# Kernel optimization log

Hardware: AMD Instinct MI355X
Metric: run time of the kernel (lower is better)

## Reference

```python
import jax, jax.numpy as jnp
import numpy as np
from jax import lax

B, L, C, H, W = 16, 8, 64, 50, 50
OC, K, PAD = 64, 3, 1
CQ = C // 16


def conv2d(x, w, b, pad):
    y = lax.conv_general_dilated(x, w, (1, 1), [(pad, pad), (pad, pad)],
                                 dimension_numbers=('NCHW', 'OIHW', 'NCHW'))
    return y + b[None, :, None, None]


def attention(x, y, q_w, q_b, k_w, k_b, v_w, v_b):
    # x, y: [b, C, 5, 5]
    b, c, h, w = x.shape
    q = conv2d(x, q_w, q_b, 1).reshape(b, -1, h * w)   # [b, CQ, N]
    kk = conv2d(y, k_w, k_b, 1).reshape(b, -1, h * w)  # [b, CQ, N]
    attn = jax.nn.softmax(jnp.einsum('bcn,bcm->bnm', q, kk), axis=-1)  # [b, Nq, Nk]
    v = conv2d(y, v_w, v_b, 1).reshape(b, c, h * w)    # [b, C, N]
    out = jnp.einsum('bcm,bnm->bcn', v, attn)          # bmm(V, attn^T)
    return out.reshape(b, c, h, w)


def setup_inputs():
    key = jax.random.key(0)
    ks = jax.random.split(key, 15)
    s = 0.05
    return {
        'x': jax.random.normal(ks[0], (B, L, C, H, W), jnp.float32),
        'weight': jax.random.normal(ks[1], (OC, C, K, K), jnp.float32) * s,
        'bias': jax.random.normal(ks[2], (OC,), jnp.float32) * s,
        'init_w': jax.random.normal(ks[3], (C, C, 3, 3), jnp.float32) * s,
        'init_b': jax.random.normal(ks[4], (C,), jnp.float32) * s,
        'q_w': jax.random.normal(ks[5], (CQ, C, 3, 3), jnp.float32) * s,
        'q_b': jax.random.normal(ks[6], (CQ,), jnp.float32) * s,
        'k_w': jax.random.normal(ks[7], (CQ, C, 3, 3), jnp.float32) * s,
        'k_b': jax.random.normal(ks[8], (CQ,), jnp.float32) * s,
        'v_w': jax.random.normal(ks[9], (C, C, 3, 3), jnp.float32) * s,
        'v_b': jax.random.normal(ks[10], (C,), jnp.float32) * s,
        'tconv_w': jax.random.normal(ks[11], (C, C), jnp.float32) * s,  # 1x1x1 Conv3d C->C
        'tconv_b': jax.random.normal(ks[12], (C,), jnp.float32) * s,
        'fc_w': jax.random.normal(ks[13], (C,), jnp.float32) * s,       # 1x1x1 Conv3d C->1
        'fc_b': jax.random.normal(ks[14], (), jnp.float32) * s,
    }


def reference(x, weight, bias, init_w, init_b, q_w, q_b, k_w, k_b, v_w, v_b,
              tconv_w, tconv_b, fc_w, fc_b):
    b, l, c, h, w = x.shape
    # --- generateweight ---
    xet = jnp.transpose(x, (0, 2, 1, 3, 4))  # [b, c, l, h, w]
    # AdaptiveMaxPool3d((None,5,5)); h,w multiples of 5 -> exact reshape max
    pooled = xet.reshape(b, c, l, 5, h // 5, 5, w // 5).max((4, 6))  # [b,c,l,5,5]
    seq = jnp.moveaxis(pooled, 2, 0)  # [l, b, c, 5, 5]
    prior0 = conv2d(seq[0], init_w, init_b, 1)

    def step(prior, xt):
        new = attention(prior, xt, q_w, q_b, k_w, k_b, v_w, v_b)
        return new, new

    _, allp = lax.scan(step, prior0, seq)            # [l, b, c, 5, 5]
    avg = jnp.moveaxis(allp, 0, 2).mean((3, 4))      # AdaptiveAvgPool3d -> [b, c, l]
    calib = jnp.einsum('oc,bcl->bol', tconv_w, avg) + tconv_b[None, :, None]  # [b,c,l]
    scale = 1.0 + jnp.transpose(calib, (0, 2, 1))    # [b, l, c]
    # finalweight[b,l,o,i,kh,kw] = weight[o,i,kh,kw] * scale[b,l,i]
    fw = weight[None, None] * scale[:, :, None, :, None, None]
    fc_out = jnp.einsum('c,bcl->bl', fc_w, avg) + fc_b  # [b, l]
    fb = bias[None, None, :] * (1.0 + fc_out)[:, :, None]  # [b, l, oc]
    # --- grouped conv with groups = b*l ---
    xg = x.reshape(1, b * l * c, h, w)
    wg = fw.reshape(b * l * OC, c, K, K)
    out = lax.conv_general_dilated(xg, wg, (1, 1), [(PAD, PAD), (PAD, PAD)],
                                   feature_group_count=b * l,
                                   dimension_numbers=('NCHW', 'OIHW', 'NCHW'))
    out = out.reshape(b * l, OC, out.shape[-2], out.shape[-1])
    out = out + fb.reshape(b * l, OC)[:, :, None, None]
    return out
```

## Files before the change

### kernel.cpp

```cpp
#include <hip/hip_runtime.h>

typedef short s16x8 __attribute__((ext_vector_type(8)));
typedef float f32x4 __attribute__((ext_vector_type(4)));
typedef unsigned int u32x4 __attribute__((ext_vector_type(4)));

__device__ __forceinline__ unsigned short bf16r(float f) {
  unsigned int u = __float_as_uint(f);
  u += 0x7fffu + ((u >> 16) & 1u);
  return (unsigned short)(u >> 16);
}
__device__ __forceinline__ float bf_lo(unsigned int u) {
  return __uint_as_float(u << 16);
}
__device__ __forceinline__ float bf_hi(unsigned int u) {
  return __uint_as_float(u & 0xffff0000u);
}


__global__ __launch_bounds__(256) void poolprep2_kernel(
    const float* __restrict__ x, float* __restrict__ pooled,
    unsigned short* __restrict__ xs) {
  const int blk = blockIdx.x;
  const int g = blk / 10;
  const int rem = blk % 10;
  const int band = rem >> 1;
  const int chalf = rem & 1;
  const int ch0 = chalf * 4;
  const float* xg = x + (size_t)g * 160000;
  unsigned short* xsg = xs + (size_t)g * (52 * 52 * 64);
  __shared__ float pm2[32 * 250];
  const int tid = threadIdx.x;

  for (int task = tid; task < 1000; task += 256) {
    int chunk4 = task & 3;
    int rest = task >> 2;
    int xpair = rest % 25;
    int r = rest / 25;
    int y = band * 10 + r;
    int chunk = ch0 + chunk4;
    const float* base = xg + (chunk * 8) * 2500 + y * 50 + xpair * 2;
    float2 v[8];
#pragma unroll
    for (int k = 0; k < 8; ++k) v[k] = *(const float2*)(base + k * 2500);
#pragma unroll
    for (int k = 0; k < 8; ++k)
      pm2[(chunk4 * 8 + k) * 250 + r * 25 + xpair] = fmaxf(v[k].x, v[k].y);
    uint4 a, b;
    a.x = (unsigned)bf16r(v[0].x) | ((unsigned)bf16r(v[1].x) << 16);
    a.y = (unsigned)bf16r(v[2].x) | ((unsigned)bf16r(v[3].x) << 16);
    a.z = (unsigned)bf16r(v[4].x) | ((unsigned)bf16r(v[5].x) << 16);
    a.w = (unsigned)bf16r(v[6].x) | ((unsigned)bf16r(v[7].x) << 16);
    b.x = (unsigned)bf16r(v[0].y) | ((unsigned)bf16r(v[1].y) << 16);
    b.y = (unsigned)bf16r(v[2].y) | ((unsigned)bf16r(v[3].y) << 16);
    b.z = (unsigned)bf16r(v[4].y) | ((unsigned)bf16r(v[5].y) << 16);
    b.w = (unsigned)bf16r(v[6].y) | ((unsigned)bf16r(v[7].y) << 16);
    int xx = xpair * 2;
    *(uint4*)&xsg[(((y + 1) * 52) + (xx + 1)) * 64 + chunk * 8] = a;
    *(uint4*)&xsg[(((y + 1) * 52) + (xx + 2)) * 64 + chunk * 8] = b;
  }
  uint4 z4;
  z4.x = 0; z4.y = 0; z4.z = 0; z4.w = 0;
  for (int task = tid; task < 80; task += 256) {
    int chunk4 = task & 3;
    int rest = task >> 2;
    int col = (rest & 1) ? 51 : 0;
    int r = rest >> 1;
    int y = band * 10 + r;
    *(uint4*)&xsg[(((y + 1) * 52) + col) * 64 + (ch0 + chunk4) * 8] = z4;
  }
  if (band == 0) {
    for (int task = tid; task < 208; task += 256)
      *(uint4*)&xsg[(task >> 2) * 64 + (ch0 + (task & 3)) * 8] = z4;
  }
  if (band == 4) {
    for (int task = tid; task < 208; task += 256)
      *(uint4*)&xsg[(51 * 52 + (task >> 2)) * 64 + (ch0 + (task & 3)) * 8] = z4;
  }
  __syncthreads();
  if (tid < 160) {
    int c_local = tid / 5, ox = tid % 5;
    const float* pr = &pm2[c_local * 250 + ox * 5];
    float m = -1e30f;
#pragma unroll
    for (int r = 0; r < 10; ++r) {
#pragma unroll
      for (int xp = 0; xp < 5; ++xp) m = fmaxf(m, pr[r * 25 + xp]);
    }
    int c_g = chalf * 32 + c_local;
    pooled[(size_t)g * 1600 + c_g * 25 + band * 5 + ox] = m;
  }
}

__device__ __forceinline__ void conv_pass2(
    const unsigned short* in_s, const unsigned short* __restrict__ wg,
    f32x4 acc[4][4], int ikk, int wave, int lane, int l15, int l4) {
#pragma unroll
  for (int dy = 0; dy < 3; ++dy) {
    const int rr = wave + dy;
#pragma unroll
    for (int dx = 0; dx < 3; ++dx) {
      const int tap = dy * 3 + dx;
      s16x8 a[4], bfr[4];
#pragma unroll
      for (int mf = 0; mf < 4; ++mf)
        a[mf] = *reinterpret_cast<const s16x8*>(
            wg + ((((tap * 2 + ikk) * 4 + mf) * 64 + lane) << 3));
#pragma unroll
      for (int nf = 0; nf < 4; ++nf) {
        int cc = nf * 16 + l15 + dx;
        int slot = l4 ^ ((cc >> 1) & 3);
        bfr[nf] = *reinterpret_cast<const s16x8*>(
            &in_s[((rr * 66 + cc) << 5) + (slot << 3)]);
      }
#pragma unroll
      for (int mf = 0; mf < 4; ++mf)
#pragma unroll
        for (int nf = 0; nf < 4; ++nf)
          acc[mf][nf] = __builtin_amdgcn_mfma_f32_16x16x32_bf16(
              a[mf], bfr[nf], acc[mf][nf], 0, 0, 0);
    }
  }
}

__global__ __launch_bounds__(256, 4) void conv_main_fast2(
    const unsigned short* __restrict__ xs, const unsigned short* __restrict__ wt3,
    const float* __restrict__ fb_g, float* __restrict__ out) {
  const int g = blockIdx.x & 127;
  const int band = blockIdx.x >> 7;
  const int y0 = band * 4;
  const int tid = threadIdx.x;
  __shared__ __align__(16) unsigned short in_s[6 * 66 * 32];
  __shared__ float fb_s[64];
  if (tid < 64) fb_s[tid] = fb_g[g * 64 + tid];

  const unsigned short* xsg = xs + (size_t)g * (52 * 52 * 64);
  const unsigned short* wg = wt3 + (size_t)g * 36864;
  const int wave = tid >> 6, lane = tid & 63;
  const int l15 = lane & 15, l4 = lane >> 4;
  const int yrow = y0 + wave;

  f32x4 acc[4][4];
  f32x4 z = {0.f, 0.f, 0.f, 0.f};
#pragma unroll
  for (int mf = 0; mf < 4; ++mf)
#pragma unroll
    for (int nf = 0; nf < 4; ++nf) acc[mf][nf] = z;

  for (int task = tid; task < 1584; task += 256) {
    int slot = task & 3;
    int c = (task >> 2) % 66;
    int r = (task >> 2) / 66;
    int py = y0 + r;
    int srcSub = slot ^ ((c >> 1) & 3);
    const unsigned short* src = xsg + ((size_t)(py * 52 + c) * 64 + srcSub * 8);
    unsigned short* ldsb = in_s + (size_t)(task & ~63) * 8;
    __builtin_amdgcn_global_load_lds(
        (const __attribute__((address_space(1))) void*)src,
        (__attribute__((address_space(3))) void*)ldsb, 16, 0, 0);
  }
  __syncthreads();
  if (yrow < 50) conv_pass2(in_s, wg, acc, 0, wave, lane, l15, l4);
  __syncthreads();
  for (int task = tid; task < 1584; task += 256) {
    int slot = task & 3;
    int c = (task >> 2) % 66;
    int r = (task >> 2) / 66;
    int py = y0 + r;
    int srcSub = slot ^ ((c >> 1) & 3);
    const unsigned short* src = xsg + ((size_t)(py * 52 + c) * 64 + 32 + srcSub * 8);
    unsigned short* ldsb = in_s + (size_t)(task & ~63) * 8;
    __builtin_amdgcn_global_load_lds(
        (const __attribute__((address_space(1))) void*)src,
        (__attribute__((address_space(3))) void*)ldsb, 16, 0, 0);
  }
  __syncthreads();
  if (yrow < 50) {
    conv_pass2(in_s, wg, acc, 1, wave, lane, l15, l4);
    float* og = out + (size_t)g * 64 * 2500 + yrow * 50;
#pragma unroll
    for (int mf = 0; mf < 4; ++mf) {
#pragma unroll
      for (int r = 0; r < 4; ++r) {
        int o = mf * 16 + l4 * 4 + r;
        float fbv = fb_s[o];
#pragma unroll
        for (int nf = 0; nf < 4; ++nf) {
          int xx = nf * 16 + l15;
          if (xx < 50) og[(size_t)o * 2500 + xx] = acc[mf][nf][r] + fbv;
        }
      }
    }
  }
}

__global__ __launch_bounds__(256) void calwt_kernel(
    const float* __restrict__ avgg, const float* __restrict__ tconvw,
    const float* __restrict__ tconvb, const float* __restrict__ fcw,
    const float* __restrict__ fcb, const float* __restrict__ bias,
    const float* __restrict__ w, float* __restrict__ fb_g,
    unsigned short* __restrict__ wt3) {
  const int g = blockIdx.x;
  const int tid = threadIdx.x;
  __shared__ float tcw_s[64 * 65];
  __shared__ float av[64];
  __shared__ float sc[64];
  for (int idx = tid; idx < 4096; idx += 256)
    tcw_s[(idx >> 6) * 65 + (idx & 63)] = tconvw[idx];
  if (tid < 64) av[tid] = avgg[g * 64 + tid];
  __syncthreads();
  if (tid < 64) {
    int o = tid;
    float cal = tconvb[o];
#pragma unroll
    for (int c = 0; c < 64; ++c) cal += tcw_s[o * 65 + c] * av[c];
    sc[o] = 1.0f + cal;
    float part = fcw[o] * av[o];
#pragma unroll
    for (int off = 32; off; off >>= 1) part += __shfl_down(part, off);
    float fc = __shfl(part, 0) + fcb[0];
    fb_g[g * 64 + o] = bias[o] * (1.0f + fc);
  }
  __syncthreads();
  unsigned short* outg = wt3 + (size_t)g * 36864;
  for (int idx = tid; idx < 36864; idx += 256) {
    int j = idx & 7;
    int lane = (idx >> 3) & 63;
    int mf = (idx >> 9) & 3;
    int ik = (idx >> 11) & 1;
    int tap = idx >> 12;
    int o = mf * 16 + (lane & 15);
    int i = ik * 32 + 8 * (lane >> 4) + j;
    outg[idx] = bf16r(w[((o * 64) + i) * 9 + tap] * sc[i]);
  }
}


__device__ __forceinline__ void conv64core(const float* pool_s,
                                           const float* __restrict__ wgt,
                                           float* red, int tid) {
  int co = tid & 63, qd = tid >> 6;
  float acc[25];
#pragma unroll
  for (int n = 0; n < 25; ++n) acc[n] = 0.f;
  for (int ci = qd * 16; ci < qd * 16 + 16; ++ci) {
    float in[25];
#pragma unroll
    for (int n = 0; n < 25; ++n) in[n] = pool_s[ci * 25 + n];
    float w9[9];
#pragma unroll
    for (int tp = 0; tp < 9; ++tp) w9[tp] = wgt[(co * 64 + ci) * 9 + tp];
#pragma unroll
    for (int n = 0; n < 25; ++n) {
      int y = n / 5, xx = n % 5;
#pragma unroll
      for (int dy = 0; dy < 3; ++dy) {
        int yy = y + dy - 1;
        if (yy < 0 || yy > 4) continue;
#pragma unroll
        for (int dx = 0; dx < 3; ++dx) {
          int xc = xx + dx - 1;
          if (xc < 0 || xc > 4) continue;
          acc[n] += in[yy * 5 + xc] * w9[dy * 3 + dx];
        }
      }
    }
  }
#pragma unroll
  for (int n = 0; n < 25; ++n) red[(qd * 64 + co) * 25 + n] = acc[n];
  __syncthreads();
}

__global__ __launch_bounds__(256) void convB2_kernel(
    const float* __restrict__ pooled, const float* __restrict__ vw,
    const float* __restrict__ vb, const float* __restrict__ kw,
    const float* __restrict__ kb, const float* __restrict__ iw,
    const float* __restrict__ ib, unsigned short* __restrict__ vbg,
    float* __restrict__ kk4g, float* __restrict__ p28g) {
  const int blk = blockIdx.x;
  __shared__ float pool_s[1600];
  __shared__ float red[6400];
  const int tid = threadIdx.x;
  for (int idx = tid; idx < 1600; idx += 256) pool_s[idx] = pooled[blk * 1600 + idx];
  __syncthreads();

  conv64core(pool_s, vw, red, tid);
  {
    unsigned short* dst = vbg + (size_t)blk * 2560;
    for (int idx = tid; idx < 1600; idx += 256) {
      float s = red[idx] + red[1600 + idx] + red[3200 + idx] + red[4800 + idx];
      dst[(idx / 25) * 40 + idx % 25] = bf16r(s + vb[idx / 25]);
    }
    for (int idx = tid; idx < 960; idx += 256)
      dst[(idx / 15) * 40 + 25 + idx % 15] = 0;
  }
  __syncthreads();

  {
    int co = tid & 3, ci = tid >> 2;
    float acc[25];
#pragma unroll
    for (int n = 0; n < 25; ++n) acc[n] = 0.f;
    float in[25];
#pragma unroll
    for (int n = 0; n < 25; ++n) in[n] = pool_s[ci * 25 + n];
    float w9[9];
#pragma unroll
    for (int tp = 0; tp < 9; ++tp) w9[tp] = kw[(co * 64 + ci) * 9 + tp];
#pragma unroll
    for (int n = 0; n < 25; ++n) {
      int y = n / 5, xx = n % 5;
#pragma unroll
      for (int dy = 0; dy < 3; ++dy) {
        int yy = y + dy - 1;
        if (yy < 0 || yy > 4) continue;
#pragma unroll
        for (int dx = 0; dx < 3; ++dx) {
          int xc = xx + dx - 1;
          if (xc < 0 || xc > 4) continue;
          acc[n] += in[yy * 5 + xc] * w9[dy * 3 + dx];
        }
      }
    }
#pragma unroll
    for (int n = 0; n < 25; ++n) red[(ci * 4 + co) * 25 + n] = acc[n];
  }
  __syncthreads();
  if (tid < 100) {
    int co = tid / 25, m = tid % 25;
    float s = 0.f;
    for (int c = 0; c < 64; ++c) s += red[(c * 4 + co) * 25 + m];
    kk4g[blk * 100 + m * 4 + co] = s + kb[co];
  }
  __syncthreads();

  if ((blk & 7) == 0) {
    conv64core(pool_s, iw, red, tid);
    float* dst = p28g + (size_t)(blk >> 3) * 1792;
    for (int idx = tid; idx < 1600; idx += 256) {
      float s = red[idx] + red[1600 + idx] + red[3200 + idx] + red[4800 + idx];
      dst[(idx / 25) * 28 + idx % 25] = s + ib[idx / 25];
    }
  }
}


__global__ __launch_bounds__(256) void scan4_kernel(
    const unsigned short* __restrict__ vbg, const float* __restrict__ kk4g,
    const float* __restrict__ p28g, const float* __restrict__ qw,
    const float* __restrict__ qb, float* __restrict__ avgg) {
  const int b = blockIdx.x;
  const int tid = threadIdx.x;
  __shared__ __align__(16) unsigned short v_bf[8 * 64 * 40];
  __shared__ __align__(16) unsigned short attn_bf[25 * 32];
  __shared__ float p_s[64 * 28];
  __shared__ float red[100 * 68];
  __shared__ f32x4 kk4_s[8 * 25];
  __shared__ float qw_s[2304];
  __shared__ float avgp[256];
  __shared__ float qb_s[4];

  {
    const u32x4* vs = (const u32x4*)(vbg + (size_t)b * 20480);
    u32x4* vd = (u32x4*)v_bf;
    for (int i = tid; i < 2560; i += 256) vd[i] = vs[i];
    const f32x4* ks = (const f32x4*)(kk4g + b * 800);
    for (int i = tid; i < 200; i += 256) kk4_s[i] = ks[i];
    const f32x4* ps = (const f32x4*)(p28g + (size_t)b * 1792);
    f32x4* pd = (f32x4*)p_s;
    for (int i = tid; i < 448; i += 256) pd[i] = ps[i];
    const f32x4* qs = (const f32x4*)qw;
    f32x4* qd = (f32x4*)qw_s;
    for (int i = tid; i < 576; i += 256) qd[i] = qs[i];
    if (tid < 4) qb_s[tid] = qb[tid];
  }
  __syncthreads();

  const int qco = tid & 3, qci = tid >> 2;
  float qwr[9];
#pragma unroll
  for (int tp = 0; tp < 9; ++tp) qwr[tp] = qw_s[(qco * 64 + qci) * 9 + tp];

#pragma unroll 1
  for (int l = 0; l < 8; ++l) {
    {
      f32x4 i4[7];
      const f32x4* pr = (const f32x4*)&p_s[qci * 28];
#pragma unroll
      for (int j = 0; j < 7; ++j) i4[j] = pr[j];
      float in[25];
#pragma unroll
      for (int n = 0; n < 25; ++n) in[n] = i4[n >> 2][n & 3];
      float acc[25];
#pragma unroll
      for (int n = 0; n < 25; ++n) acc[n] = 0.f;
#pragma unroll
      for (int n = 0; n < 25; ++n) {
        int y = n / 5, xx = n % 5;
#pragma unroll
        for (int dy = 0; dy < 3; ++dy) {
          int yy = y + dy - 1;
          if (yy < 0 || yy > 4) continue;
#pragma unroll
          for (int dx = 0; dx < 3; ++dx) {
            int xc = xx + dx - 1;
            if (xc < 0 || xc > 4) continue;
            acc[n] += in[yy * 5 + xc] * qwr[dy * 3 + dx];
          }
        }
      }
#pragma unroll
      for (int n = 0; n < 25; ++n) red[(qco * 25 + n) * 68 + qci] = acc[n];
    }
    if (l > 0 && tid < 64) {
      f32x4 a4 = *(const f32x4*)&avgp[tid * 4];
      avgg[(b * 8 + l - 1) * 64 + tid] = (a4[0] + a4[1] + a4[2] + a4[3]) * 0.04f;
    }
    __syncthreads();

    if (tid < 25) {
      const int n = tid;
      float qv[4];
#pragma unroll
      for (int co = 0; co < 4; ++co) {
        const f32x4* rp = (const f32x4*)&red[(co * 25 + n) * 68];
        float s = 0.f;
#pragma unroll
        for (int j = 0; j < 16; ++j) {
          f32x4 r4 = rp[j];
          s += r4[0] + r4[1] + r4[2] + r4[3];
        }
        qv[co] = s + qb_s[co];
      }
      const f32x4* kk = &kk4_s[l * 25];
      float row[25];
      float mx = -1e30f;
#pragma unroll
      for (int m = 0; m < 25; ++m) {
        f32x4 k4 = kk[m];
        float s = qv[0] * k4[0] + qv[1] * k4[1] + qv[2] * k4[2] + qv[3] * k4[3];
        row[m] = s;
        mx = fmaxf(mx, s);
      }
      float sm = 0.f;
#pragma unroll
      for (int m = 0; m < 25; ++m) {
        float e = __expf(row[m] - mx);
        row[m] = e;
        sm += e;
      }
      float inv = 1.0f / sm;
      unsigned int w16[16];
#pragma unroll
      for (int j = 0; j < 16; ++j) {
        float lo = (2 * j < 25) ? row[2 * j] * inv : 0.f;
        float hi = (2 * j + 1 < 25) ? row[2 * j + 1] * inv : 0.f;
        w16[j] = (unsigned)bf16r(lo) | ((unsigned)bf16r(hi) << 16);
      }
      u32x4* ad = (u32x4*)&attn_bf[n * 32];
      u32x4 d0 = {w16[0], w16[1], w16[2], w16[3]};
      u32x4 d1 = {w16[4], w16[5], w16[6], w16[7]};
      u32x4 d2 = {w16[8], w16[9], w16[10], w16[11]};
      u32x4 d3 = {w16[12], w16[13], w16[14], w16[15]};
      ad[0] = d0; ad[1] = d1; ad[2] = d2; ad[3] = d3;
    }
    __syncthreads();

    {
      const int c = tid & 63, grp = tid >> 6;
      const u32x4* vr = (const u32x4*)&v_bf[(l * 64 + c) * 40];
      u32x4 vv[4];
#pragma unroll
      for (int j = 0; j < 4; ++j) vv[j] = vr[j];
      float vf[25];
#pragma unroll
      for (int m = 0; m < 25; ++m) {
        unsigned int u = vv[m >> 3][(m >> 1) & 3];
        vf[m] = (m & 1) ? bf_hi(u) : bf_lo(u);
      }
      float partial = 0.f;
      for (int n = grp; n < 25; n += 4) {
        const u32x4* ar = (const u32x4*)&attn_bf[n * 32];
        u32x4 aa[4];
#pragma unroll
        for (int j = 0; j < 4; ++j) aa[j] = ar[j];
        float acc = 0.f;
#pragma unroll
        for (int m = 0; m < 25; ++m) {
          unsigned int u = aa[m >> 3][(m >> 1) & 3];
          float a = (m & 1) ? bf_hi(u) : bf_lo(u);
          acc += vf[m] * a;
        }
        p_s[c * 28 + n] = acc;
        partial += acc;
      }
      avgp[(c << 2) + grp] = partial;
    }
    __syncthreads();
  }
  if (tid < 64) {
    f32x4 a4 = *(const f32x4*)&avgp[tid * 4];
    avgg[(b * 8 + 7) * 64 + tid] = (a4[0] + a4[1] + a4[2] + a4[3]) * 0.04f;
  }
}


__global__ __launch_bounds__(256) void pool_kernel(const float* __restrict__ x,
                                                   float* __restrict__ pooled) {
  const int blk = blockIdx.x;
  const float* plane = x + (size_t)blk * 2500;
  __shared__ float pmax[250];
  const int t = threadIdx.x;
  if (t < 250) {
    int r = t / 5, cc = t % 5;
    const float* row = plane + r * 50 + cc * 10;
    float m = row[0];
#pragma unroll
    for (int j = 1; j < 10; ++j) m = fmaxf(m, row[j]);
    pmax[r * 5 + cc] = m;
  }
  __syncthreads();
  if (t < 25) {
    int pr = t / 5, cc = t % 5;
    float m = pmax[(pr * 10) * 5 + cc];
#pragma unroll
    for (int rr = 1; rr < 10; ++rr) m = fmaxf(m, pmax[(pr * 10 + rr) * 5 + cc]);
    pooled[(size_t)blk * 25 + t] = m;
  }
}

__global__ __launch_bounds__(256) void wt_kernel(const float* __restrict__ w,
                                                 unsigned short* __restrict__ wt2) {
  int idx = blockIdx.x * 256 + threadIdx.x;
  if (idx >= 36864) return;
  int j = idx & 7;
  int lane = (idx >> 3) & 63;
  int mf = (idx >> 9) & 3;
  int ik = (idx >> 11) & 1;
  int tap = idx >> 12;
  int o = mf * 16 + (lane & 15);
  int i = ik * 32 + 8 * (lane >> 4) + j;
  wt2[idx] = bf16r(w[((o * 64) + i) * 9 + tap]);
}

__global__ __launch_bounds__(256) void conv_main(
    const float* __restrict__ x, const unsigned short* __restrict__ wt2,
    const float* __restrict__ scale_g, const float* __restrict__ fb_g,
    float* __restrict__ out) {
  const int g = blockIdx.x & 127;
  const int band = blockIdx.x >> 7;
  const int y0 = band * 4;
  const int tid = threadIdx.x;
  __shared__ unsigned short in_s[6 * 66 * 64];
  __shared__ float scale_s[64], fb_s[64];
  if (tid < 64) {
    scale_s[tid] = scale_g[g * 64 + tid];
    fb_s[tid] = fb_g[g * 64 + tid];
  }
  __syncthreads();
  const float* xg = x + (size_t)g * 160000;
  for (int task = tid; task < 3168; task += 256) {
    int c = task % 66;
    int rc = task / 66;
    int r = rc >> 3;
    int chunk = rc & 7;
    int y = y0 - 1 + r;
    int xi = c - 1;
    unsigned int p0 = 0, p1 = 0, p2 = 0, p3 = 0;
    if (y >= 0 && y < 50 && xi >= 0 && xi < 50) {
      const float* px = xg + chunk * 8 * 2500 + y * 50 + xi;
      float f0 = px[0] * scale_s[chunk * 8 + 0];
      float f1 = px[2500] * scale_s[chunk * 8 + 1];
      float f2 = px[5000] * scale_s[chunk * 8 + 2];
      float f3 = px[7500] * scale_s[chunk * 8 + 3];
      float f4 = px[10000] * scale_s[chunk * 8 + 4];
      float f5 = px[12500] * scale_s[chunk * 8 + 5];
      float f6 = px[15000] * scale_s[chunk * 8 + 6];
      float f7 = px[17500] * scale_s[chunk * 8 + 7];
      p0 = (unsigned)bf16r(f0) | ((unsigned)bf16r(f1) << 16);
      p1 = (unsigned)bf16r(f2) | ((unsigned)bf16r(f3) << 16);
      p2 = (unsigned)bf16r(f4) | ((unsigned)bf16r(f5) << 16);
      p3 = (unsigned)bf16r(f6) | ((unsigned)bf16r(f7) << 16);
    }
    int chS = chunk ^ (c & 7);
    uint4* dst = (uint4*)&in_s[((r * 66 + c) << 6) + (chS << 3)];
    uint4 u4;
    u4.x = p0; u4.y = p1; u4.z = p2; u4.w = p3;
    *dst = u4;
  }
  __syncthreads();
  const int wave = tid >> 6, lane = tid & 63;
  const int l15 = lane & 15, l4 = lane >> 4;
  const int yrow = y0 + wave;
  if (yrow < 50) {
    f32x4 acc[4][4];
    f32x4 z = {0.f, 0.f, 0.f, 0.f};
#pragma unroll
    for (int mf = 0; mf < 4; ++mf)
#pragma unroll
      for (int nf = 0; nf < 4; ++nf) acc[mf][nf] = z;
#pragma unroll
    for (int dy = 0; dy < 3; ++dy) {
      const int rr = wave + dy;
#pragma unroll
      for (int dx = 0; dx < 3; ++dx) {
        const int tap = dy * 3 + dx;
#pragma unroll
        for (int ik = 0; ik < 2; ++ik) {
          s16x8 a[4], bfr[4];
#pragma unroll
          for (int mf = 0; mf < 4; ++mf)
            a[mf] = *reinterpret_cast<const s16x8*>(
                wt2 + ((((tap * 2 + ik) * 4 + mf) * 64 + lane) << 3));
#pragma unroll
          for (int nf = 0; nf < 4; ++nf) {
            int cc = nf * 16 + l15 + dx;
            int chS = (ik * 4 + l4) ^ (cc & 7);
            bfr[nf] = *reinterpret_cast<const s16x8*>(
                &in_s[((rr * 66 + cc) << 6) + (chS << 3)]);
          }
#pragma unroll
          for (int mf = 0; mf < 4; ++mf)
#pragma unroll
            for (int nf = 0; nf < 4; ++nf)
              acc[mf][nf] = __builtin_amdgcn_mfma_f32_16x16x32_bf16(
                  a[mf], bfr[nf], acc[mf][nf], 0, 0, 0);
        }
      }
    }
    float* og = out + (size_t)g * 64 * 2500 + yrow * 50;
#pragma unroll
    for (int mf = 0; mf < 4; ++mf) {
#pragma unroll
      for (int r = 0; r < 4; ++r) {
        int o = mf * 16 + l4 * 4 + r;
        float fbv = fb_s[o];
#pragma unroll
        for (int nf = 0; nf < 4; ++nf) {
          int xx = nf * 16 + l15;
          if (xx < 50) og[(size_t)o * 2500 + xx] = acc[mf][nf][r] + fbv;
        }
      }
    }
  }
}

__global__ __launch_bounds__(256) void calib_kernel(
    const float* __restrict__ avgg, const float* __restrict__ tconvw,
    const float* __restrict__ tconvb, const float* __restrict__ fcw,
    const float* __restrict__ fcb, const float* __restrict__ bias,
    float* __restrict__ scale_g, float* __restrict__ fb_g) {
  const int tid = threadIdx.x;
  const int wave = tid >> 6, o = tid & 63;
  const int bl = blockIdx.x * 4 + wave;
  __shared__ float tcw_s[64 * 65];
  __shared__ float avgl[4][64];
  for (int idx = tid; idx < 4096; idx += 256)
    tcw_s[(idx >> 6) * 65 + (idx & 63)] = tconvw[idx];
  avgl[wave][o] = avgg[bl * 64 + o];
  __syncthreads();
  float cal = tconvb[o];
  const float* av = avgl[wave];
#pragma unroll
  for (int c = 0; c < 64; ++c) cal += tcw_s[o * 65 + c] * av[c];
  scale_g[bl * 64 + o] = 1.0f + cal;
  float part = fcw[o] * av[o];
#pragma unroll
  for (int off = 32; off; off >>= 1) part += __shfl_down(part, off);
  float fc = __shfl(part, 0) + fcb[0];
  fb_g[bl * 64 + o] = bias[o] * (1.0f + fc);
}

extern "C" void kernel_launch(void* const* d_in, const int* in_sizes, int n_in,
                              void* d_out, int out_size, void* d_ws, size_t ws_size,
                              hipStream_t stream) {
  const float* x       = (const float*)d_in[0];
  const float* weight  = (const float*)d_in[1];
  const float* bias    = (const float*)d_in[2];
  const float* init_w  = (const float*)d_in[3];
  const float* init_b  = (const float*)d_in[4];
  const float* q_w     = (const float*)d_in[5];
  const float* q_b     = (const float*)d_in[6];
  const float* k_w     = (const float*)d_in[7];
  const float* k_b     = (const float*)d_in[8];
  const float* v_w     = (const float*)d_in[9];
  const float* v_b     = (const float*)d_in[10];
  const float* tconv_w = (const float*)d_in[11];
  const float* tconv_b = (const float*)d_in[12];
  const float* fc_w    = (const float*)d_in[13];
  const float* fc_b    = (const float*)d_in[14];
  float* out = (float*)d_out;

  float* ws = (float*)d_ws;
  float* pooled = ws;
  unsigned short* vbg = (unsigned short*)(ws + 204800);
  float* kk4g   = ws + 368640;
  float* p28g   = ws + 381440;
  float* scaleg = ws + 410112;
  float* fbg    = ws + 418304;
  float* avgg   = ws + 426496;
  unsigned short* wt3 = (unsigned short*)(ws + 434688);
  unsigned short* xsb = wt3 + 4718592;

  const size_t NEED_FAST = 55543808ull;

  if (ws_size >= NEED_FAST) {
    poolprep2_kernel<<<1280, 256, 0, stream>>>(x, pooled, xsb);
    convB2_kernel<<<128, 256, 0, stream>>>(pooled, v_w, v_b, k_w, k_b, init_w,
                                           init_b, vbg, kk4g, p28g);
    scan4_kernel<<<16, 256, 0, stream>>>(vbg, kk4g, p28g, q_w, q_b, avgg);
    calwt_kernel<<<128, 256, 0, stream>>>(avgg, tconv_w, tconv_b, fc_w, fc_b, bias,
                                          weight, fbg, wt3);
    conv_main_fast2<<<13 * 128, 256, 0, stream>>>(xsb, wt3, fbg, out);
  } else {
    unsigned short* wt2 = (unsigned short*)(ws + 434688);
    pool_kernel<<<8192, 256, 0, stream>>>(x, pooled);
    wt_kernel<<<144, 256, 0, stream>>>(weight, wt2);
    convB2_kernel<<<128, 256, 0, stream>>>(pooled, v_w, v_b, k_w, k_b, init_w,
                                           init_b, vbg, kk4g, p28g);
    scan4_kernel<<<16, 256, 0, stream>>>(vbg, kk4g, p28g, q_w, q_b, avgg);
    calib_kernel<<<32, 256, 0, stream>>>(avgg, tconv_w, tconv_b, fc_w, fc_b, bias,
                                         scaleg, fbg);
    conv_main<<<13 * 128, 256, 0, stream>>>(x, wt2, scaleg, fbg, out);
  }
}
```

Measured before the change: 154.6 us.

## Overlap bf16 padded-input prep with the serial attention scan kernel

Splits the fused pool+bf16-prep kernel so the first kernel only computes the max-pool, and moves the padded bf16 NHWC input conversion into extra blocks of the scan kernel. The 16-block latency-bound scan then shares the GPU with the 1280 bandwidth-bound prep blocks instead of running alone. The scan is also restructured to reduce the q-conv partials with wave shuffles instead of a large LDS reduction buffer, and to read V straight from global memory per step instead of staging all of it in LDS. The scan blocks may now compete with prep blocks for bandwidth and CUs, and the input tensor is read twice, once for pooling and once for prep.

```diff
diff --git a/kernel.cpp b/kernel.cpp
--- a/kernel.cpp
+++ b/kernel.cpp
@@ -17,9 +17,8 @@
 }
 
 
-__global__ __launch_bounds__(256) void poolprep2_kernel(
-    const float* __restrict__ x, float* __restrict__ pooled,
-    unsigned short* __restrict__ xs) {
+__global__ __launch_bounds__(256) void pool3_kernel(
+    const float* __restrict__ x, float* __restrict__ pooled) {
   const int blk = blockIdx.x;
   const int g = blk / 10;
   const int rem = blk % 10;
@@ -27,7 +26,6 @@
   const int chalf = rem & 1;
   const int ch0 = chalf * 4;
   const float* xg = x + (size_t)g * 160000;
-  unsigned short* xsg = xs + (size_t)g * (52 * 52 * 64);
   __shared__ float pm2[32 * 250];
   const int tid = threadIdx.x;
 
@@ -45,6 +43,44 @@
 #pragma unroll
     for (int k = 0; k < 8; ++k)
       pm2[(chunk4 * 8 + k) * 250 + r * 25 + xpair] = fmaxf(v[k].x, v[k].y);
+  }
+  __syncthreads();
+  if (tid < 160) {
+    int c_local = tid / 5, ox = tid % 5;
+    const float* pr = &pm2[c_local * 250 + ox * 5];
+    float m = -1e30f;
+#pragma unroll
+    for (int r = 0; r < 10; ++r) {
+#pragma unroll
+      for (int xp = 0; xp < 5; ++xp) m = fmaxf(m, pr[r * 25 + xp]);
+    }
+    int c_g = chalf * 32 + c_local;
+    pooled[(size_t)g * 1600 + c_g * 25 + band * 5 + ox] = m;
+  }
+}
+
+__device__ __forceinline__ void xsprep_block(int blk, const float* __restrict__ x,
+                                             unsigned short* __restrict__ xs) {
+  const int g = blk / 10;
+  const int rem = blk % 10;
+  const int band = rem >> 1;
+  const int chalf = rem & 1;
+  const int ch0 = chalf * 4;
+  const float* xg = x + (size_t)g * 160000;
+  unsigned short* xsg = xs + (size_t)g * (52 * 52 * 64);
+  const int tid = threadIdx.x;
+
+  for (int task = tid; task < 1000; task += 256) {
+    int chunk4 = task & 3;
+    int rest = task >> 2;
+    int xpair = rest % 25;
+    int r = rest / 25;
+    int y = band * 10 + r;
+    int chunk = ch0 + chunk4;
+    const float* base = xg + (chunk * 8) * 2500 + y * 50 + xpair * 2;
+    float2 v[8];
+#pragma unroll
+    for (int k = 0; k < 8; ++k) v[k] = *(const float2*)(base + k * 2500);
     uint4 a, b;
     a.x = (unsigned)bf16r(v[0].x) | ((unsigned)bf16r(v[1].x) << 16);
     a.y = (unsigned)bf16r(v[2].x) | ((unsigned)bf16r(v[3].x) << 16);
@@ -76,18 +112,167 @@
     for (int task = tid; task < 208; task += 256)
       *(uint4*)&xsg[(51 * 52 + (task >> 2)) * 64 + (ch0 + (task & 3)) * 8] = z4;
   }
-  __syncthreads();
-  if (tid < 160) {
-    int c_local = tid / 5, ox = tid % 5;
-    const float* pr = &pm2[c_local * 250 + ox * 5];
-    float m = -1e30f;
-#pragma unroll
-    for (int r = 0; r < 10; ++r) {
-#pragma unroll
-      for (int xp = 0; xp < 5; ++xp) m = fmaxf(m, pr[r * 25 + xp]);
-    }
-    int c_g = chalf * 32 + c_local;
-    pooled[(size_t)g * 1600 + c_g * 25 + band * 5 + ox] = m;
+}
+
+__global__ __launch_bounds__(256) void scanx2_kernel(
+    const unsigned short* __restrict__ vbg, const float* __restrict__ kk4g,
+    const float* __restrict__ p28g, const float* __restrict__ qw,
+    const float* __restrict__ qb, float* __restrict__ avgg,
+    const float* __restrict__ x, unsigned short* __restrict__ xs) {
+  if (blockIdx.x >= 16) {
+    xsprep_block(blockIdx.x - 16, x, xs);
+    return;
+  }
+  __shared__ __align__(16) unsigned short attn_bf[25 * 32];
+  __shared__ float p_s[64 * 28];
+  __shared__ f32x4 kk4_s[8 * 25];
+  __shared__ float q_s[100];
+  __shared__ float avgp[256];
+  __shared__ float qb_s[4];
+
+  const int b = blockIdx.x;
+  const int tid = threadIdx.x;
+  const int co = tid >> 6, ci = tid & 63;
+
+  {
+    const f32x4* ks = (const f32x4*)(kk4g + b * 800);
+    for (int i = tid; i < 200; i += 256) kk4_s[i] = ks[i];
+    const f32x4* ps = (const f32x4*)(p28g + (size_t)b * 1792);
+    f32x4* pd = (f32x4*)p_s;
+    for (int i = tid; i < 448; i += 256) pd[i] = ps[i];
+    if (tid < 4) qb_s[tid] = qb[tid];
+  }
+  float qwr[9];
+#pragma unroll
+  for (int t = 0; t < 9; ++t) qwr[t] = qw[(co * 64 + ci) * 9 + t];
+  __syncthreads();
+
+#pragma unroll 1
+  for (int l = 0; l < 8; ++l) {
+    u32x4 vv[4];
+    {
+      const u32x4* vr =
+          (const u32x4*)(vbg + (size_t)(b * 8 + l) * 2560 + ci * 40);
+#pragma unroll
+      for (int j = 0; j < 4; ++j) vv[j] = vr[j];
+    }
+
+    float acc[25];
+    {
+      f32x4 i4[7];
+      const f32x4* pr = (const f32x4*)&p_s[ci * 28];
+#pragma unroll
+      for (int j = 0; j < 7; ++j) i4[j] = pr[j];
+      float in[25];
+#pragma unroll
+      for (int n = 0; n < 25; ++n) in[n] = i4[n >> 2][n & 3];
+#pragma unroll
+      for (int n = 0; n < 25; ++n) acc[n] = 0.f;
+#pragma unroll
+      for (int n = 0; n < 25; ++n) {
+        int y = n / 5, xx = n % 5;
+#pragma unroll
+        for (int dy = 0; dy < 3; ++dy) {
+          int yy = y + dy - 1;
+          if (yy < 0 || yy > 4) continue;
+#pragma unroll
+          for (int dx = 0; dx < 3; ++dx) {
+            int xc = xx + dx - 1;
+            if (xc < 0 || xc > 4) continue;
+            acc[n] += in[yy * 5 + xc] * qwr[dy * 3 + dx];
+          }
+        }
+      }
+#pragma unroll
+      for (int n = 0; n < 25; ++n) {
+        float v = acc[n];
+        v += __shfl_xor(v, 1);
+        v += __shfl_xor(v, 2);
+        v += __shfl_xor(v, 4);
+        v += __shfl_xor(v, 8);
+        v += __shfl_xor(v, 16);
+        v += __shfl_xor(v, 32);
+        acc[n] = v;
+      }
+    }
+    if (l > 0 && tid < 64) {
+      f32x4 a4 = *(const f32x4*)&avgp[tid * 4];
+      avgg[(b * 8 + l - 1) * 64 + tid] = (a4[0] + a4[1] + a4[2] + a4[3]) * 0.04f;
+    }
+    if (ci == 0) {
+#pragma unroll
+      for (int n = 0; n < 25; ++n) q_s[co * 25 + n] = acc[n] + qb_s[co];
+    }
+    __syncthreads();
+
+    if (tid < 25) {
+      const int n = tid;
+      float q0 = q_s[n], q1 = q_s[25 + n], q2 = q_s[50 + n], q3 = q_s[75 + n];
+      const f32x4* kk = &kk4_s[l * 25];
+      float row[25];
+      float mx = -1e30f;
+#pragma unroll
+      for (int m = 0; m < 25; ++m) {
+        f32x4 k4 = kk[m];
+        float s = q0 * k4[0] + q1 * k4[1] + q2 * k4[2] + q3 * k4[3];
+        row[m] = s;
+        mx = fmaxf(mx, s);
+      }
+      float sm = 0.f;
+#pragma unroll
+      for (int m = 0; m < 25; ++m) {
+        float e = __expf(row[m] - mx);
+        row[m] = e;
+        sm += e;
+      }
+      float inv = 1.0f / sm;
+      unsigned int w16[16];
+#pragma unroll
+      for (int j = 0; j < 16; ++j) {
+        float lo = (2 * j < 25) ? row[2 * j] * inv : 0.f;
+        float hi = (2 * j + 1 < 25) ? row[2 * j + 1] * inv : 0.f;
+        w16[j] = (unsigned)bf16r(lo) | ((unsigned)bf16r(hi) << 16);
+      }
+      u32x4* ad = (u32x4*)&attn_bf[n * 32];
+      u32x4 d0 = {w16[0], w16[1], w16[2], w16[3]};
+      u32x4 d1 = {w16[4], w16[5], w16[6], w16[7]};
+      u32x4 d2 = {w16[8], w16[9], w16[10], w16[11]};
+      u32x4 d3 = {w16[12], w16[13], w16[14], w16[15]};
+      ad[0] = d0; ad[1] = d1; ad[2] = d2; ad[3] = d3;
+    }
+    __syncthreads();
+
+    {
+      const int c = ci, grp = co;
+      float vf[25];
+#pragma unroll
+      for (int m = 0; m < 25; ++m) {
+        unsigned int u = vv[m >> 3][(m >> 1) & 3];
+        vf[m] = (m & 1) ? bf_hi(u) : bf_lo(u);
+      }
+      float partial = 0.f;
+      for (int n = grp; n < 25; n += 4) {
+        const u32x4* ar = (const u32x4*)&attn_bf[n * 32];
+        u32x4 aa[4];
+#pragma unroll
+        for (int j = 0; j < 4; ++j) aa[j] = ar[j];
+        float acc2 = 0.f;
+#pragma unroll
+        for (int m = 0; m < 25; ++m) {
+          unsigned int u = aa[m >> 3][(m >> 1) & 3];
+          float a = (m & 1) ? bf_hi(u) : bf_lo(u);
+          acc2 += vf[m] * a;
+        }
+        p_s[c * 28 + n] = acc2;
+        partial += acc2;
+      }
+      avgp[(c << 2) + grp] = partial;
+    }
+    __syncthreads();
+  }
+  if (tid < 64) {
+    f32x4 a4 = *(const f32x4*)&avgp[tid * 4];
+    avgg[(b * 8 + 7) * 64 + tid] = (a4[0] + a4[1] + a4[2] + a4[3]) * 0.04f;
   }
 }
 
@@ -340,166 +525,6 @@
       float s = red[idx] + red[1600 + idx] + red[3200 + idx] + red[4800 + idx];
       dst[(idx / 25) * 28 + idx % 25] = s + ib[idx / 25];
     }
-  }
-}
-
-
-__global__ __launch_bounds__(256) void scan4_kernel(
-    const unsigned short* __restrict__ vbg, const float* __restrict__ kk4g,
-    const float* __restrict__ p28g, const float* __restrict__ qw,
-    const float* __restrict__ qb, float* __restrict__ avgg) {
-  const int b = blockIdx.x;
-  const int tid = threadIdx.x;
-  __shared__ __align__(16) unsigned short v_bf[8 * 64 * 40];
-  __shared__ __align__(16) unsigned short attn_bf[25 * 32];
-  __shared__ float p_s[64 * 28];
-  __shared__ float red[100 * 68];
-  __shared__ f32x4 kk4_s[8 * 25];
-  __shared__ float qw_s[2304];
-  __shared__ float avgp[256];
-  __shared__ float qb_s[4];
-
-  {
-    const u32x4* vs = (const u32x4*)(vbg + (size_t)b * 20480);
-    u32x4* vd = (u32x4*)v_bf;
-    for (int i = tid; i < 2560; i += 256) vd[i] = vs[i];
-    const f32x4* ks = (const f32x4*)(kk4g + b * 800);
-    for (int i = tid; i < 200; i += 256) kk4_s[i] = ks[i];
-    const f32x4* ps = (const f32x4*)(p28g + (size_t)b * 1792);
-    f32x4* pd = (f32x4*)p_s;
-    for (int i = tid; i < 448; i += 256) pd[i] = ps[i];
-    const f32x4* qs = (const f32x4*)qw;
-    f32x4* qd = (f32x4*)qw_s;
-    for (int i = tid; i < 576; i += 256) qd[i] = qs[i];
-    if (tid < 4) qb_s[tid] = qb[tid];
-  }
-  __syncthreads();
-
-  const int qco = tid & 3, qci = tid >> 2;
-  float qwr[9];
-#pragma unroll
-  for (int tp = 0; tp < 9; ++tp) qwr[tp] = qw_s[(qco * 64 + qci) * 9 + tp];
-
-#pragma unroll 1
-  for (int l = 0; l < 8; ++l) {
-    {
-      f32x4 i4[7];
-      const f32x4* pr = (const f32x4*)&p_s[qci * 28];
-#pragma unroll
-      for (int j = 0; j < 7; ++j) i4[j] = pr[j];
-      float in[25];
-#pragma unroll
-      for (int n = 0; n < 25; ++n) in[n] = i4[n >> 2][n & 3];
-      float acc[25];
-#pragma unroll
-      for (int n = 0; n < 25; ++n) acc[n] = 0.f;
-#pragma unroll
-      for (int n = 0; n < 25; ++n) {
-        int y = n / 5, xx = n % 5;
-#pragma unroll
-        for (int dy = 0; dy < 3; ++dy) {
-          int yy = y + dy - 1;
-          if (yy < 0 || yy > 4) continue;
-#pragma unroll
-          for (int dx = 0; dx < 3; ++dx) {
-            int xc = xx + dx - 1;
-            if (xc < 0 || xc > 4) continue;
-            acc[n] += in[yy * 5 + xc] * qwr[dy * 3 + dx];
-          }
-        }
-      }
-#pragma unroll
-      for (int n = 0; n < 25; ++n) red[(qco * 25 + n) * 68 + qci] = acc[n];
-    }
-    if (l > 0 && tid < 64) {
-      f32x4 a4 = *(const f32x4*)&avgp[tid * 4];
-      avgg[(b * 8 + l - 1) * 64 + tid] = (a4[0] + a4[1] + a4[2] + a4[3]) * 0.04f;
-    }
-    __syncthreads();
-
-    if (tid < 25) {
-      const int n = tid;
-      float qv[4];
-#pragma unroll
-      for (int co = 0; co < 4; ++co) {
-        const f32x4* rp = (const f32x4*)&red[(co * 25 + n) * 68];
-        float s = 0.f;
-#pragma unroll
-        for (int j = 0; j < 16; ++j) {
-          f32x4 r4 = rp[j];
-          s += r4[0] + r4[1] + r4[2] + r4[3];
-        }
-        qv[co] = s + qb_s[co];
-      }
-      const f32x4* kk = &kk4_s[l * 25];
-      float row[25];
-      float mx = -1e30f;
-#pragma unroll
-      for (int m = 0; m < 25; ++m) {
-        f32x4 k4 = kk[m];
-        float s = qv[0] * k4[0] + qv[1] * k4[1] + qv[2] * k4[2] + qv[3] * k4[3];
-        row[m] = s;
-        mx = fmaxf(mx, s);
-      }
-      float sm = 0.f;
-#pragma unroll
-      for (int m = 0; m < 25; ++m) {
-        float e = __expf(row[m] - mx);
-        row[m] = e;
-        sm += e;
-      }
-      float inv = 1.0f / sm;
-      unsigned int w16[16];
-#pragma unroll
-      for (int j = 0; j < 16; ++j) {
-        float lo = (2 * j < 25) ? row[2 * j] * inv : 0.f;
-        float hi = (2 * j + 1 < 25) ? row[2 * j + 1] * inv : 0.f;
-        w16[j] = (unsigned)bf16r(lo) | ((unsigned)bf16r(hi) << 16);
-      }
-      u32x4* ad = (u32x4*)&attn_bf[n * 32];
-      u32x4 d0 = {w16[0], w16[1], w16[2], w16[3]};
-      u32x4 d1 = {w16[4], w16[5], w16[6], w16[7]};
-      u32x4 d2 = {w16[8], w16[9], w16[10], w16[11]};
-      u32x4 d3 = {w16[12], w16[13], w16[14], w16[15]};
-      ad[0] = d0; ad[1] = d1; ad[2] = d2; ad[3] = d3;
-    }
-    __syncthreads();
-
-    {
-      const int c = tid & 63, grp = tid >> 6;
-      const u32x4* vr = (const u32x4*)&v_bf[(l * 64 + c) * 40];
-      u32x4 vv[4];
-#pragma unroll
-      for (int j = 0; j < 4; ++j) vv[j] = vr[j];
-      float vf[25];
-#pragma unroll
-      for (int m = 0; m < 25; ++m) {
-        unsigned int u = vv[m >> 3][(m >> 1) & 3];
-        vf[m] = (m & 1) ? bf_hi(u) : bf_lo(u);
-      }
-      float partial = 0.f;
-      for (int n = grp; n < 25; n += 4) {
-        const u32x4* ar = (const u32x4*)&attn_bf[n * 32];
-        u32x4 aa[4];
-#pragma unroll
-        for (int j = 0; j < 4; ++j) aa[j] = ar[j];
-        float acc = 0.f;
-#pragma unroll
-        for (int m = 0; m < 25; ++m) {
-          unsigned int u = aa[m >> 3][(m >> 1) & 3];
-          float a = (m & 1) ? bf_hi(u) : bf_lo(u);
-          acc += vf[m] * a;
-        }
-        p_s[c * 28 + n] = acc;
-        partial += acc;
-      }
-      avgp[(c << 2) + grp] = partial;
-    }
-    __syncthreads();
-  }
-  if (tid < 64) {
-    f32x4 a4 = *(const f32x4*)&avgp[tid * 4];
-    avgg[(b * 8 + 7) * 64 + tid] = (a4[0] + a4[1] + a4[2] + a4[3]) * 0.04f;
   }
 }
 
@@ -704,10 +729,11 @@
   const size_t NEED_FAST = 55543808ull;
 
   if (ws_size >= NEED_FAST) {
-    poolprep2_kernel<<<1280, 256, 0, stream>>>(x, pooled, xsb);
+    pool3_kernel<<<1280, 256, 0, stream>>>(x, pooled);
     convB2_kernel<<<128, 256, 0, stream>>>(pooled, v_w, v_b, k_w, k_b, init_w,
                                            init_b, vbg, kk4g, p28g);
-    scan4_kernel<<<16, 256, 0, stream>>>(vbg, kk4g, p28g, q_w, q_b, avgg);
+    scanx2_kernel<<<16 + 1280, 256, 0, stream>>>(vbg, kk4g, p28g, q_w, q_b, avgg,
+                                                 x, xsb);
     calwt_kernel<<<128, 256, 0, stream>>>(avgg, tconv_w, tconv_b, fc_w, fc_b, bias,
                                           weight, fbg, wt3);
     conv_main_fast2<<<13 * 128, 256, 0, stream>>>(xsb, wt3, fbg, out);
@@ -717,7 +743,8 @@
     wt_kernel<<<144, 256, 0, stream>>>(weight, wt2);
     convB2_kernel<<<128, 256, 0, stream>>>(pooled, v_w, v_b, k_w, k_b, init_w,
                                            init_b, vbg, kk4g, p28g);
-    scan4_kernel<<<16, 256, 0, stream>>>(vbg, kk4g, p28g, q_w, q_b, avgg);
+    scanx2_kernel<<<16, 256, 0, stream>>>(vbg, kk4g, p28g, q_w, q_b, avgg,
+                                          x, (unsigned short*)0);
     calib_kernel<<<32, 256, 0, stream>>>(avgg, tconv_w, tconv_b, fc_w, fc_b, bias,
                                          scaleg, fbg);
     conv_main<<<13 * 128, 256, 0, stream>>>(x, wt2, scaleg, fbg, out);
```

After: 158.6 us. +2.6%, slower.
